# Kernel tuning notes

Measured on AMD Instinct MI355X. Metric: run time of the kernel, lower is better.

Reference implementation:

```python
import jax, jax.numpy as jnp
import numpy as np

E = 8            # n_expert
K = 2            # n_expert_per_token
C = 2048         # n_embd
I = 1408         # moe_intermediate_size
IS = I * 2       # shared expert intermediate (n_shared_expert=2)
B, T = 2, 2048


def setup_inputs() -> dict:
    key = jax.random.key(0)
    ks = jax.random.split(key, 9)
    s = 0.02
    return {
        "x": jax.random.normal(ks[0], (B, T, C), dtype=jnp.float32),
        "gate_w": jax.random.normal(ks[1], (E, C), dtype=jnp.float32) * s,
        # expert MLP weights, torch Linear convention (out_features, in_features)
        "w1": jax.random.normal(ks[2], (E, I, C), dtype=jnp.float32) * s,  # fc_1
        "w2": jax.random.normal(ks[3], (E, I, C), dtype=jnp.float32) * s,  # fc_2
        "w3": jax.random.normal(ks[4], (E, C, I), dtype=jnp.float32) * s,  # proj
        # shared expert
        "sw1": jax.random.normal(ks[5], (IS, C), dtype=jnp.float32) * s,
        "sw2": jax.random.normal(ks[6], (IS, C), dtype=jnp.float32) * s,
        "sw3": jax.random.normal(ks[7], (C, IS), dtype=jnp.float32) * s,
    }


def reference(x, gate_w, w1, w2, w3, sw1, sw2, sw3):
    Bq, Tq, Cq = x.shape
    xf = x.reshape(-1, Cq)  # [N, C], N = B*T

    # top-k routing: softmax in fp32, then top-k probs per token
    logits = xf @ gate_w.T                                   # [N, E]
    probs = jax.nn.softmax(logits.astype(jnp.float32), axis=-1)
    topk_p, topk_i = jax.lax.top_k(probs, K)                 # [N, K]
    # combine weights: comb[n, e] = sum_k topk_p[n,k] * (topk_i[n,k] == e)
    comb = (jax.nn.one_hot(topk_i, E, dtype=jnp.float32)
            * topk_p[..., None]).sum(axis=1).astype(x.dtype)  # [N, E]

    # per-expert gated-SiLU MLP (batched over experts via einsum)
    h1 = jnp.einsum('nc,eic->eni', xf, w1)                   # [E, N, I]
    h2 = jnp.einsum('nc,eic->eni', xf, w2)                   # [E, N, I]
    h = jax.nn.silu(h1) * h2
    eo = jnp.einsum('eni,eci->enc', h, w3)                   # [E, N, C]

    # weighted scatter-combine
    y = jnp.einsum('enc,ne->nc', eo, comb).reshape(Bq, Tq, Cq)

    # shared expert on the residual input
    sh = (jax.nn.silu(xf @ sw1.T) * (xf @ sw2.T)) @ sw3.T    # [N, C]
    return y + sh.reshape(Bq, Tq, Cq)
```

## Files before the change

### kernel.cpp

```cpp
#include <hip/hip_runtime.h>
#include <stdint.h>

#define N_TOK 4096
#define CDIM  2048
#define NEXP  8
#define IDIM  1408
#define ISDIM 2816
#define CAP   2048
#define ICAT  2816
#define SCAT  5632

typedef __attribute__((ext_vector_type(8))) short bf16x8;
typedef __attribute__((ext_vector_type(4))) float f32x4;

#define GLOAD16(gp, lp) __builtin_amdgcn_global_load_lds( \
    (const __attribute__((address_space(1))) void*)(gp),  \
    (__attribute__((address_space(3))) void*)(lp), 16, 0, 0)

__device__ __forceinline__ unsigned short f2bf(float f) {
  union { float f; unsigned u; } c; c.f = f;
  return (unsigned short)((c.u + 0x7FFFu + ((c.u >> 16) & 1u)) >> 16);
}
__device__ __forceinline__ float bf2f(unsigned short h) {
  union { unsigned u; float f; } c; c.u = (unsigned)h << 16;
  return c.f;
}

__device__ __forceinline__ int xcd_swizzle(int orig, int nwg) {
  int q = nwg >> 3, r = nwg & 7;
  int xcd = orig & 7, idx = orig >> 3;
  return (xcd < r ? xcd * (q + 1) : r * (q + 1) + (xcd - r) * q) + idx;
}

__global__ __launch_bounds__(256) void cvt_all(
    const float* __restrict__ x, const float* __restrict__ w1,
    const float* __restrict__ w2, const float* __restrict__ w3,
    const float* __restrict__ sw1, const float* __restrict__ sw2,
    const float* __restrict__ sw3,
    unsigned short* __restrict__ xb, unsigned short* __restrict__ wcat,
    unsigned short* __restrict__ w3b, unsigned short* __restrict__ swcat,
    unsigned short* __restrict__ sw3b) {
  const int b = blockIdx.x;
  const int t = threadIdx.x;
  const float* src;
  unsigned short* dst;
  if (b < 4096) {
    src = x + (size_t)b * 2048;  dst = xb + (size_t)b * 2048;
  } else if (b < 15360) {
    size_t o = (size_t)(b - 4096) * 2048;  src = w3 + o;  dst = w3b + o;
  } else if (b < 18176) {
    size_t o = (size_t)(b - 15360) * 2048; src = sw3 + o; dst = sw3b + o;
  } else if (b < 40704) {
    int g = b - 18176;
    int e = g / 2816, r = g - e * 2816;
    int dr;
    if (r < 1408) { src = w1 + ((size_t)e * 1408 + r) * 2048; dr = (r >> 7) * 256 + (r & 127); }
    else { int r2 = r - 1408; src = w2 + ((size_t)e * 1408 + r2) * 2048; dr = (r2 >> 7) * 256 + 128 + (r2 & 127); }
    dst = wcat + ((size_t)e * ICAT + dr) * 2048;
  } else {
    int g = b - 40704;
    int dr;
    if (g < 2816) {
      int zn = g >= 1408, rr = g - zn * 1408;
      src = sw1 + (size_t)g * 2048;
      dr = zn * 2816 + (rr >> 7) * 256 + (rr & 127);
    } else {
      int r = g - 2816;
      int zn = r >= 1408, rr = r - zn * 1408;
      src = sw2 + (size_t)r * 2048;
      dr = zn * 2816 + (rr >> 7) * 256 + 128 + (rr & 127);
    }
    dst = swcat + (size_t)dr * 2048;
  }
  size_t i = (size_t)t * 8;
  float4 v0 = *(const float4*)(src + i);
  float4 v1 = *(const float4*)(src + i + 4);
  bf16x8 o;
  o[0] = (short)f2bf(v0.x); o[1] = (short)f2bf(v0.y);
  o[2] = (short)f2bf(v0.z); o[3] = (short)f2bf(v0.w);
  o[4] = (short)f2bf(v1.x); o[5] = (short)f2bf(v1.y);
  o[6] = (short)f2bf(v1.z); o[7] = (short)f2bf(v1.w);
  *(bf16x8*)(dst + i) = o;
}

__global__ __launch_bounds__(64) void routing_kernel(
    const float* __restrict__ x, const float* __restrict__ gw,
    int* __restrict__ counts, int* __restrict__ list,
    int* __restrict__ slot_of, float* __restrict__ wts) {
  const int n = blockIdx.x;
  const int lane = threadIdx.x;
  const float* xr = x + (size_t)n * CDIM;
  float s[NEXP];
#pragma unroll
  for (int e = 0; e < NEXP; e++) s[e] = 0.f;
  for (int c = lane; c < CDIM; c += 64) {
    float xv = xr[c];
#pragma unroll
    for (int e = 0; e < NEXP; e++) s[e] += xv * gw[e * CDIM + c];
  }
#pragma unroll
  for (int e = 0; e < NEXP; e++) {
    float v = s[e];
    for (int o = 32; o > 0; o >>= 1) v += __shfl_down(v, o);
    s[e] = v;
  }
  if (lane == 0) {
    float mx = s[0];
#pragma unroll
    for (int e = 1; e < NEXP; e++) mx = fmaxf(mx, s[e]);
    float p[NEXP], sum = 0.f;
#pragma unroll
    for (int e = 0; e < NEXP; e++) { p[e] = __expf(s[e] - mx); sum += p[e]; }
    int i0 = 0;
#pragma unroll
    for (int e = 1; e < NEXP; e++) if (p[e] > p[i0]) i0 = e;
    int i1 = (i0 == 0) ? 1 : 0;
#pragma unroll
    for (int e = 0; e < NEXP; e++) if (e != i0 && p[e] > p[i1]) i1 = e;
    float inv = 1.f / sum;
    int s0 = atomicAdd(&counts[i0], 1);
    int s1 = atomicAdd(&counts[i1], 1);
    if (s0 < CAP) list[i0 * CAP + s0] = n; else s0 = 0;
    if (s1 < CAP) list[i1 * CAP + s1] = n; else s1 = 0;
    slot_of[n * 2]     = i0 * CAP + s0;
    slot_of[n * 2 + 1] = i1 * CAP + s1;
    wts[n * 2]     = p[i0] * inv;
    wts[n * 2 + 1] = p[i1] * inv;
  }
}

template <int PHASE>
__global__ __launch_bounds__(512) void moe_gemm(
    const unsigned short* __restrict__ xb,
    const unsigned short* __restrict__ swcat,
    const unsigned short* __restrict__ wcat,
    unsigned short* __restrict__ hs_out,
    unsigned short* __restrict__ he_out,
    const unsigned short* __restrict__ hs,
    const unsigned short* __restrict__ sw3b,
    const unsigned short* __restrict__ he,
    const unsigned short* __restrict__ w3b,
    float* __restrict__ ysf,
    unsigned short* __restrict__ eo,
    const int* __restrict__ list,
    const int* __restrict__ counts) {
  const int z = blockIdx.z;
  const unsigned short *A, *B;
  unsigned short* O = nullptr;
  float* Of = nullptr;
  int Ka, ldo;
  int cnt = 1 << 30;
  const int* lst = nullptr;
  int Mt, Nt;
  bool gath = false;
  if (PHASE == 1) {
    Mt = 8; Nt = 11; Ka = CDIM;
    if (z < 4) {
      int zm = z >> 1, zn = z & 1;
      A = xb + (size_t)zm * 2048 * CDIM;
      B = swcat + (size_t)zn * 2816 * CDIM;
      O = hs_out + (size_t)zm * 2048 * ISDIM + (size_t)zn * 1408;
      ldo = ISDIM;
    } else {
      int e = z - 4;
      cnt = counts[e]; if (cnt > CAP) cnt = CAP;
      lst = list + e * CAP;
      gath = true;
      A = xb;
      B = wcat + (size_t)e * ICAT * CDIM;
      O = he_out + (size_t)e * CAP * IDIM;
      ldo = IDIM;
    }
  } else {
    Mt = 8; Nt = 8;
    if (z < 2) {
      Ka = ISDIM;
      A = hs + (size_t)z * 2048 * ISDIM;
      B = sw3b;
      Of = ysf + (size_t)z * 2048 * CDIM;
      ldo = CDIM;
    } else {
      int e = z - 2;
      cnt = counts[e]; if (cnt > CAP) cnt = CAP;
      Ka = IDIM;
      A = he + (size_t)e * CAP * IDIM;
      B = w3b + (size_t)e * CDIM * IDIM;
      O = eo + (size_t)e * CAP * CDIM;
      ldo = CDIM;
    }
  }
  const int wg = xcd_swizzle(blockIdx.x, Mt * Nt);
  const int mt = wg % Mt, nt = wg / Mt;
  if (mt * 256 >= cnt) return;

  __shared__ __align__(16) char lds[2][2][2][16384];

  const int tid = threadIdx.x;
  const int srow = tid >> 2;
  const int c16  = (tid & 3) << 4;
  const int scol = c16 ^ (((srow >> 1) & 3) << 4);
  const char* aS[2];
  const char* bS[2];
#pragma unroll
  for (int j = 0; j < 2; j++) {
    int ar = mt * 256 + j * 128 + srow;
    if (PHASE == 1 && gath) ar = (ar < cnt) ? lst[ar] : lst[0];
    aS[j] = (const char*)A + (size_t)ar * Ka * 2 + scol;
    int br = nt * 256 + j * 128 + srow;
    bS[j] = (const char*)B + (size_t)br * Ka * 2 + scol;
  }
  auto stageA = [&](int buf, int kt, int h) {
    size_t kb = (size_t)kt * 128 + (size_t)(h << 6);
    char* aD = &lds[buf][0][h][0] + tid * 16;
    GLOAD16(aS[0] + kb, aD);
    GLOAD16(aS[1] + kb, aD + 8192);
  };
  auto stageB = [&](int buf, int kt, int h) {
    size_t kb = (size_t)kt * 128 + (size_t)(h << 6);
    char* bD = &lds[buf][1][h][0] + tid * 16;
    GLOAD16(bS[0] + kb, bD);
    GLOAD16(bS[1] + kb, bD + 8192);
  };

  const int lane = tid & 63, wid = tid >> 6;
  const int wr = wid >> 2, wc = wid & 3;
  const int lrow = lane & 15;
  const int klane = (lane >> 4) << 4;
  const int rsw = ((lrow >> 1) & 3) << 4;
  const int aOff = (wr * 128 + lrow) * 64 + (klane ^ rsw);
  const int bOff = (wc * 64 + lrow) * 64 + (klane ^ rsw);

  f32x4 acc[8][4];
#pragma unroll
  for (int mf = 0; mf < 8; mf++)
#pragma unroll
    for (int nf = 0; nf < 4; nf++) acc[mf][nf] = (f32x4){0.f, 0.f, 0.f, 0.f};

  stageA(0, 0, 0); stageB(0, 0, 0);
  stageA(0, 0, 1); stageB(0, 0, 1);
  stageA(1, 1, 0); stageB(1, 1, 0);
  asm volatile("s_waitcnt vmcnt(8)" ::: "memory");
  __builtin_amdgcn_s_barrier();

#define MFMA_ALL                                                               \
  _Pragma("unroll")                                                            \
  for (int nf = 0; nf < 4; nf++)                                               \
    _Pragma("unroll")                                                          \
    for (int m = 0; m < 8; m++)                                                \
      acc[m][nf] = __builtin_amdgcn_mfma_f32_16x16x32_bf16(                    \
          aR[m], bR[nf], acc[m][nf], 0, 0, 0);

  const int ntk = Ka >> 6;
  for (int t = 0; t < ntk; t++) {
    const int p = t & 1;
    const char* aK0 = &lds[p][0][0][0];
    const char* aK1 = &lds[p][0][1][0];
    const char* bK0 = &lds[p][1][0][0];
    const char* bK1 = &lds[p][1][1][0];
    bf16x8 aR[8], bR[4];
#pragma unroll
    for (int i = 0; i < 8; i++) aR[i] = *(const bf16x8*)(aK0 + aOff + i * 1024);
#pragma unroll
    for (int i = 0; i < 4; i++) bR[i] = *(const bf16x8*)(bK0 + bOff + i * 1024);
    if (t + 1 < ntk) {
      stageA(p ^ 1, t + 1, 1);
      stageB(p ^ 1, t + 1, 1);
      asm volatile("s_waitcnt vmcnt(8)" ::: "memory");
    } else {
      asm volatile("s_waitcnt vmcnt(0)" ::: "memory");
    }
    __builtin_amdgcn_s_barrier();
    asm volatile("s_waitcnt lgkmcnt(0)" ::: "memory");
    __builtin_amdgcn_s_setprio(1);
    MFMA_ALL
    __builtin_amdgcn_s_setprio(0);
    __builtin_amdgcn_s_barrier();
#pragma unroll
    for (int i = 0; i < 8; i++) aR[i] = *(const bf16x8*)(aK1 + aOff + i * 1024);
#pragma unroll
    for (int i = 0; i < 4; i++) bR[i] = *(const bf16x8*)(bK1 + bOff + i * 1024);
    if (t + 2 < ntk) {
      stageA(p, t + 2, 0);
      stageB(p, t + 2, 0);
      asm volatile("s_waitcnt vmcnt(8)" ::: "memory");
    } else if (t + 1 < ntk) {
      asm volatile("s_waitcnt vmcnt(4)" ::: "memory");
    }
    __builtin_amdgcn_s_barrier();
    asm volatile("s_waitcnt lgkmcnt(0)" ::: "memory");
    __builtin_amdgcn_s_setprio(1);
    MFMA_ALL
    __builtin_amdgcn_s_setprio(0);
    __builtin_amdgcn_s_barrier();
  }
#undef MFMA_ALL

  const int r4 = (lane >> 4) * 4;
  if (PHASE == 1) {
    float* ldsF = (float*)&lds[0][0][0][0];
    const int rbase = wr * 128 + r4;
    if (wc >= 2) {
      const int cb = (wc - 2) * 64;
#pragma unroll
      for (int mf = 0; mf < 8; mf++)
#pragma unroll
        for (int nf = 0; nf < 4; nf++) {
          int cc = cb + nf * 16 + lrow;
#pragma unroll
          for (int r = 0; r < 4; r++) {
            int rr = rbase + mf * 16 + r;
            ldsF[rr * 128 + (cc ^ (((rr >> 2) & 1) << 4))] = acc[mf][nf][r];
          }
        }
    }
    __syncthreads();
    if (wc < 2) {
      const int cb = wc * 64;
#pragma unroll
      for (int mf = 0; mf < 8; mf++) {
        int row0 = mt * 256 + wr * 128 + mf * 16 + r4;
#pragma unroll
        for (int nf = 0; nf < 4; nf++) {
          int cc = cb + nf * 16 + lrow;
          int col = nt * 128 + cc;
#pragma unroll
          for (int r = 0; r < 4; r++) {
            int rr = rbase + mf * 16 + r;
            float z1 = acc[mf][nf][r];
            float z2 = ldsF[rr * 128 + (cc ^ (((rr >> 2) & 1) << 4))];
            float gv = z1 / (1.f + __expf(-z1)) * z2;
            O[(size_t)(row0 + r) * ldo + col] = f2bf(gv);
          }
        }
      }
    }
  } else {
    const int rowb = mt * 256 + wr * 128;
    const int colb = nt * 256 + wc * 64;
#pragma unroll
    for (int mf = 0; mf < 8; mf++) {
      int row0 = rowb + mf * 16 + r4;
#pragma unroll
      for (int nf = 0; nf < 4; nf++) {
        int col = colb + nf * 16 + lrow;
#pragma unroll
        for (int r = 0; r < 4; r++) {
          if (z < 2)
            Of[(size_t)(row0 + r) * ldo + col] = acc[mf][nf][r];
          else
            O[(size_t)(row0 + r) * ldo + col] = f2bf(acc[mf][nf][r]);
        }
      }
    }
  }
}

__global__ __launch_bounds__(256) void combine_kernel(
    float* __restrict__ y, const float* __restrict__ ysf,
    const unsigned short* __restrict__ eo,
    const int* __restrict__ slot_of, const float* __restrict__ wts) {
  int idx = blockIdx.x * 256 + threadIdx.x;
  int n = idx >> 9;
  int c = (idx & 511) * 4;
  float4 v = *(const float4*)(ysf + (size_t)n * CDIM + c);
#pragma unroll
  for (int k = 0; k < 2; k++) {
    int slot = slot_of[n * 2 + k];
    float w = wts[n * 2 + k];
    ushort4 h = *(const ushort4*)(eo + (size_t)slot * CDIM + c);
    v.x += w * bf2f(h.x);
    v.y += w * bf2f(h.y);
    v.z += w * bf2f(h.z);
    v.w += w * bf2f(h.w);
  }
  *(float4*)(y + (size_t)n * CDIM + c) = v;
}

extern "C" void kernel_launch(void* const* d_in, const int* in_sizes, int n_in,
                              void* d_out, int out_size, void* d_ws, size_t ws_size,
                              hipStream_t stream) {
  const float* x   = (const float*)d_in[0];
  const float* gw  = (const float*)d_in[1];
  const float* w1  = (const float*)d_in[2];
  const float* w2  = (const float*)d_in[3];
  const float* w3  = (const float*)d_in[4];
  const float* sw1 = (const float*)d_in[5];
  const float* sw2 = (const float*)d_in[6];
  const float* sw3 = (const float*)d_in[7];
  float* y = (float*)d_out;

  char* ws = (char*)d_ws;
  size_t off = 0;
  auto alloc = [&](size_t b) -> void* {
    void* p = ws + off;
    off += (b + 255) & ~(size_t)255;
    return p;
  };
  unsigned short* xb    = (unsigned short*)alloc((size_t)N_TOK * CDIM * 2);
  unsigned short* wcat  = (unsigned short*)alloc((size_t)NEXP * ICAT * CDIM * 2);
  unsigned short* w3b   = (unsigned short*)alloc((size_t)NEXP * CDIM * IDIM * 2);
  unsigned short* swcat = (unsigned short*)alloc((size_t)SCAT * CDIM * 2);
  unsigned short* sw3b  = (unsigned short*)alloc((size_t)CDIM * ISDIM * 2);
  unsigned short* hs    = (unsigned short*)alloc((size_t)N_TOK * ISDIM * 2);
  unsigned short* he    = (unsigned short*)alloc((size_t)NEXP * CAP * IDIM * 2);
  float*          ysf   = (float*)alloc((size_t)N_TOK * CDIM * 4);
  int*   counts  = (int*)alloc(NEXP * 4);
  int*   list    = (int*)alloc((size_t)NEXP * CAP * 4);
  int*   slot_of = (int*)alloc((size_t)N_TOK * 2 * 4);
  float* wtsb    = (float*)alloc((size_t)N_TOK * 2 * 4);
  unsigned short* eoB = wcat;

  hipMemsetAsync(counts, 0, NEXP * 4, stream);
  routing_kernel<<<N_TOK, 64, 0, stream>>>(x, gw, counts, list, slot_of, wtsb);

  cvt_all<<<46336, 256, 0, stream>>>(x, w1, w2, w3, sw1, sw2, sw3,
                                     xb, wcat, w3b, swcat, sw3b);

  moe_gemm<1><<<dim3(88, 1, 12), 512, 0, stream>>>(
      xb, swcat, wcat, hs, he, hs, sw3b, he, w3b, ysf, eoB, list, counts);

  moe_gemm<2><<<dim3(64, 1, 10), 512, 0, stream>>>(
      xb, swcat, wcat, hs, he, hs, sw3b, he, w3b, ysf, eoB, list, counts);

  combine_kernel<<<(N_TOK * (CDIM / 4)) / 256, 256, 0, stream>>>(y, ysf, eoB, slot_of, wtsb);
}
```

Before: 622.0 us.

## Shrink MoE GEMM tiles to 128x256 with two blocks per CU

Both GEMM phases drop from 256x256 tiles with a 64-wide K step to 128x256 tiles with a 32-wide K step. The main loop becomes a simpler double-buffered pipeline, LDS use falls from 128KB to 48KB, and launch bounds now ask for two 512-thread blocks per CU. The shared-expert phase-1 launch is reorganized from four z-slices into two z-slices with 22 N tiles each. The gated-SiLU epilogue now exchanges z2 through LDS as bf16 instead of fp32. The aim is more occupancy and better latency hiding, at the cost of lower per-tile reuse, more barriers per unit of work, and a small rounding change in z2.

```diff
diff --git a/kernel.cpp b/kernel.cpp
--- a/kernel.cpp
+++ b/kernel.cpp
@@ -130,7 +130,7 @@
 }
 
 template <int PHASE>
-__global__ __launch_bounds__(512) void moe_gemm(
+__global__ __launch_bounds__(512, 2) void moe_gemm(
     const unsigned short* __restrict__ xb,
     const unsigned short* __restrict__ swcat,
     const unsigned short* __restrict__ wcat,
@@ -154,15 +154,16 @@
   int Mt, Nt;
   bool gath = false;
   if (PHASE == 1) {
-    Mt = 8; Nt = 11; Ka = CDIM;
-    if (z < 4) {
-      int zm = z >> 1, zn = z & 1;
-      A = xb + (size_t)zm * 2048 * CDIM;
-      B = swcat + (size_t)zn * 2816 * CDIM;
-      O = hs_out + (size_t)zm * 2048 * ISDIM + (size_t)zn * 1408;
+    Mt = 16; Ka = CDIM;
+    if (z < 2) {
+      Nt = 22;
+      A = xb + (size_t)z * 2048 * CDIM;
+      B = swcat;
+      O = hs_out + (size_t)z * 2048 * ISDIM;
       ldo = ISDIM;
     } else {
-      int e = z - 4;
+      Nt = 11;
+      int e = z - 2;
       cnt = counts[e]; if (cnt > CAP) cnt = CAP;
       lst = list + e * CAP;
       gath = true;
@@ -172,7 +173,7 @@
       ldo = IDIM;
     }
   } else {
-    Mt = 8; Nt = 8;
+    Mt = 16; Nt = 8;
     if (z < 2) {
       Ka = ISDIM;
       A = hs + (size_t)z * 2048 * ISDIM;
@@ -189,37 +190,33 @@
       ldo = CDIM;
     }
   }
-  const int wg = xcd_swizzle(blockIdx.x, Mt * Nt);
+  const int nwg = Mt * Nt;
+  if ((int)blockIdx.x >= nwg) return;
+  const int wg = xcd_swizzle(blockIdx.x, nwg);
   const int mt = wg % Mt, nt = wg / Mt;
-  if (mt * 256 >= cnt) return;
-
-  __shared__ __align__(16) char lds[2][2][2][16384];
+  if (mt * 128 >= cnt) return;
+
+  __shared__ __align__(16) char lds[2][24576];
 
   const int tid = threadIdx.x;
   const int srow = tid >> 2;
   const int c16  = (tid & 3) << 4;
   const int scol = c16 ^ (((srow >> 1) & 3) << 4);
-  const char* aS[2];
+  const char* aS;
   const char* bS[2];
-#pragma unroll
-  for (int j = 0; j < 2; j++) {
-    int ar = mt * 256 + j * 128 + srow;
+  {
+    int ar = mt * 128 + srow;
     if (PHASE == 1 && gath) ar = (ar < cnt) ? lst[ar] : lst[0];
-    aS[j] = (const char*)A + (size_t)ar * Ka * 2 + scol;
-    int br = nt * 256 + j * 128 + srow;
-    bS[j] = (const char*)B + (size_t)br * Ka * 2 + scol;
-  }
-  auto stageA = [&](int buf, int kt, int h) {
-    size_t kb = (size_t)kt * 128 + (size_t)(h << 6);
-    char* aD = &lds[buf][0][h][0] + tid * 16;
-    GLOAD16(aS[0] + kb, aD);
-    GLOAD16(aS[1] + kb, aD + 8192);
-  };
-  auto stageB = [&](int buf, int kt, int h) {
-    size_t kb = (size_t)kt * 128 + (size_t)(h << 6);
-    char* bD = &lds[buf][1][h][0] + tid * 16;
-    GLOAD16(bS[0] + kb, bD);
-    GLOAD16(bS[1] + kb, bD + 8192);
+    aS = (const char*)A + (size_t)ar * Ka * 2 + scol;
+    bS[0] = (const char*)B + (size_t)(nt * 256 + srow) * Ka * 2 + scol;
+    bS[1] = (const char*)B + (size_t)(nt * 256 + 128 + srow) * Ka * 2 + scol;
+  }
+  auto stage = [&](int buf, int kt) {
+    size_t kb = (size_t)kt * 64;
+    char* d = &lds[buf][0] + tid * 16;
+    GLOAD16(aS + kb, d);
+    GLOAD16(bS[0] + kb, d + 8192);
+    GLOAD16(bS[1] + kb, d + 16384);
   };
 
   const int lane = tid & 63, wid = tid >> 6;
@@ -227,89 +224,56 @@
   const int lrow = lane & 15;
   const int klane = (lane >> 4) << 4;
   const int rsw = ((lrow >> 1) & 3) << 4;
-  const int aOff = (wr * 128 + lrow) * 64 + (klane ^ rsw);
-  const int bOff = (wc * 64 + lrow) * 64 + (klane ^ rsw);
-
-  f32x4 acc[8][4];
-#pragma unroll
-  for (int mf = 0; mf < 8; mf++)
+  const int aOff = (wr * 64 + lrow) * 64 + (klane ^ rsw);
+  const int bOff = 8192 + (wc * 64 + lrow) * 64 + (klane ^ rsw);
+
+  f32x4 acc[4][4];
+#pragma unroll
+  for (int mf = 0; mf < 4; mf++)
 #pragma unroll
     for (int nf = 0; nf < 4; nf++) acc[mf][nf] = (f32x4){0.f, 0.f, 0.f, 0.f};
 
-  stageA(0, 0, 0); stageB(0, 0, 0);
-  stageA(0, 0, 1); stageB(0, 0, 1);
-  stageA(1, 1, 0); stageB(1, 1, 0);
-  asm volatile("s_waitcnt vmcnt(8)" ::: "memory");
-  __builtin_amdgcn_s_barrier();
-
-#define MFMA_ALL                                                               \
-  _Pragma("unroll")                                                            \
-  for (int nf = 0; nf < 4; nf++)                                               \
-    _Pragma("unroll")                                                          \
-    for (int m = 0; m < 8; m++)                                                \
-      acc[m][nf] = __builtin_amdgcn_mfma_f32_16x16x32_bf16(                    \
-          aR[m], bR[nf], acc[m][nf], 0, 0, 0);
-
-  const int ntk = Ka >> 6;
+  stage(0, 0);
+  stage(1, 1);
+
+  const int ntk = Ka >> 5;
   for (int t = 0; t < ntk; t++) {
-    const int p = t & 1;
-    const char* aK0 = &lds[p][0][0][0];
-    const char* aK1 = &lds[p][0][1][0];
-    const char* bK0 = &lds[p][1][0][0];
-    const char* bK1 = &lds[p][1][1][0];
-    bf16x8 aR[8], bR[4];
-#pragma unroll
-    for (int i = 0; i < 8; i++) aR[i] = *(const bf16x8*)(aK0 + aOff + i * 1024);
-#pragma unroll
-    for (int i = 0; i < 4; i++) bR[i] = *(const bf16x8*)(bK0 + bOff + i * 1024);
-    if (t + 1 < ntk) {
-      stageA(p ^ 1, t + 1, 1);
-      stageB(p ^ 1, t + 1, 1);
-      asm volatile("s_waitcnt vmcnt(8)" ::: "memory");
-    } else {
-      asm volatile("s_waitcnt vmcnt(0)" ::: "memory");
-    }
+    const char* base = lds[t & 1];
+    if (t + 1 < ntk) asm volatile("s_waitcnt vmcnt(3)" ::: "memory");
+    else             asm volatile("s_waitcnt vmcnt(0)" ::: "memory");
     __builtin_amdgcn_s_barrier();
+    bf16x8 aR[4], bR[4];
+#pragma unroll
+    for (int i = 0; i < 4; i++) aR[i] = *(const bf16x8*)(base + aOff + i * 1024);
+#pragma unroll
+    for (int i = 0; i < 4; i++) bR[i] = *(const bf16x8*)(base + bOff + i * 1024);
     asm volatile("s_waitcnt lgkmcnt(0)" ::: "memory");
+    __builtin_amdgcn_s_barrier();
+    if (t + 2 < ntk) stage(t & 1, t + 2);
     __builtin_amdgcn_s_setprio(1);
-    MFMA_ALL
+#pragma unroll
+    for (int nf = 0; nf < 4; nf++)
+#pragma unroll
+      for (int mf = 0; mf < 4; mf++)
+        acc[mf][nf] = __builtin_amdgcn_mfma_f32_16x16x32_bf16(
+            aR[mf], bR[nf], acc[mf][nf], 0, 0, 0);
     __builtin_amdgcn_s_setprio(0);
-    __builtin_amdgcn_s_barrier();
-#pragma unroll
-    for (int i = 0; i < 8; i++) aR[i] = *(const bf16x8*)(aK1 + aOff + i * 1024);
-#pragma unroll
-    for (int i = 0; i < 4; i++) bR[i] = *(const bf16x8*)(bK1 + bOff + i * 1024);
-    if (t + 2 < ntk) {
-      stageA(p, t + 2, 0);
-      stageB(p, t + 2, 0);
-      asm volatile("s_waitcnt vmcnt(8)" ::: "memory");
-    } else if (t + 1 < ntk) {
-      asm volatile("s_waitcnt vmcnt(4)" ::: "memory");
-    }
-    __builtin_amdgcn_s_barrier();
-    asm volatile("s_waitcnt lgkmcnt(0)" ::: "memory");
-    __builtin_amdgcn_s_setprio(1);
-    MFMA_ALL
-    __builtin_amdgcn_s_setprio(0);
-    __builtin_amdgcn_s_barrier();
-  }
-#undef MFMA_ALL
+  }
 
   const int r4 = (lane >> 4) * 4;
   if (PHASE == 1) {
-    float* ldsF = (float*)&lds[0][0][0][0];
-    const int rbase = wr * 128 + r4;
+    unsigned short* ldsH = (unsigned short*)&lds[0][0];
     if (wc >= 2) {
       const int cb = (wc - 2) * 64;
 #pragma unroll
-      for (int mf = 0; mf < 8; mf++)
+      for (int mf = 0; mf < 4; mf++)
 #pragma unroll
         for (int nf = 0; nf < 4; nf++) {
           int cc = cb + nf * 16 + lrow;
 #pragma unroll
           for (int r = 0; r < 4; r++) {
-            int rr = rbase + mf * 16 + r;
-            ldsF[rr * 128 + (cc ^ (((rr >> 2) & 1) << 4))] = acc[mf][nf][r];
+            int rr = wr * 64 + mf * 16 + r4 + r;
+            ldsH[rr * 128 + (cc ^ (((rr >> 2) & 7) << 4))] = f2bf(acc[mf][nf][r]);
           }
         }
     }
@@ -317,28 +281,27 @@
     if (wc < 2) {
       const int cb = wc * 64;
 #pragma unroll
-      for (int mf = 0; mf < 8; mf++) {
-        int row0 = mt * 256 + wr * 128 + mf * 16 + r4;
+      for (int mf = 0; mf < 4; mf++) {
 #pragma unroll
         for (int nf = 0; nf < 4; nf++) {
           int cc = cb + nf * 16 + lrow;
           int col = nt * 128 + cc;
 #pragma unroll
           for (int r = 0; r < 4; r++) {
-            int rr = rbase + mf * 16 + r;
+            int rr = wr * 64 + mf * 16 + r4 + r;
             float z1 = acc[mf][nf][r];
-            float z2 = ldsF[rr * 128 + (cc ^ (((rr >> 2) & 1) << 4))];
+            float z2 = bf2f(ldsH[rr * 128 + (cc ^ (((rr >> 2) & 7) << 4))]);
             float gv = z1 / (1.f + __expf(-z1)) * z2;
-            O[(size_t)(row0 + r) * ldo + col] = f2bf(gv);
+            O[(size_t)(mt * 128 + rr) * ldo + col] = f2bf(gv);
           }
         }
       }
     }
   } else {
-    const int rowb = mt * 256 + wr * 128;
+    const int rowb = mt * 128 + wr * 64;
     const int colb = nt * 256 + wc * 64;
 #pragma unroll
-    for (int mf = 0; mf < 8; mf++) {
+    for (int mf = 0; mf < 4; mf++) {
       int row0 = rowb + mf * 16 + r4;
 #pragma unroll
       for (int nf = 0; nf < 4; nf++) {
@@ -416,10 +379,10 @@
   cvt_all<<<46336, 256, 0, stream>>>(x, w1, w2, w3, sw1, sw2, sw3,
                                      xb, wcat, w3b, swcat, sw3b);
 
-  moe_gemm<1><<<dim3(88, 1, 12), 512, 0, stream>>>(
+  moe_gemm<1><<<dim3(352, 1, 10), 512, 0, stream>>>(
       xb, swcat, wcat, hs, he, hs, sw3b, he, w3b, ysf, eoB, list, counts);
 
-  moe_gemm<2><<<dim3(64, 1, 10), 512, 0, stream>>>(
+  moe_gemm<2><<<dim3(128, 1, 10), 512, 0, stream>>>(
       xb, swcat, wcat, hs, he, hs, sw3b, he, w3b, ysf, eoB, list, counts);
 
   combine_kernel<<<(N_TOK * (CDIM / 4)) / 256, 256, 0, stream>>>(y, ysf, eoB, slot_of, wtsb);
```

Measured after the change: 633.2 us. Within noise of the previous version (+1.8%).
